# Performance work log

Hardware: AMD Instinct MI355X
Metric: run time of the kernel (lower is better)

## Reference

```python
import jax, jax.numpy as jnp
import numpy as np

N = 65536        # nodes
E = 131072       # directed edges
D = 512          # emb_dim
L = 5            # num_layer
G = 512          # num graphs
EPS = 1e-5       # batchnorm eps
NUM_ATOM_TYPE, NUM_CHIRALITY = 120, 3
NUM_BOND_TYPE, NUM_BOND_DIR = 6, 3


def setup_inputs() -> dict:
    key = jax.random.key(0)
    ks = jax.random.split(key, 12)
    s = 0.02
    return {
        "x": jax.random.randint(ks[0], (N, 2), 0, 3),
        "edge_index": jax.random.randint(ks[1], (2, E), 0, N),
        "edge_attr": jax.random.randint(ks[2], (E, 2), 0, 3),
        "batch": jnp.sort(jax.random.randint(ks[3], (N,), 0, G)),
        "x_emb1": jax.random.normal(ks[4], (NUM_ATOM_TYPE, D), jnp.float32) * s,
        "x_emb2": jax.random.normal(ks[5], (NUM_CHIRALITY, D), jnp.float32) * s,
        "e_emb1": jax.random.normal(ks[6], (L, NUM_BOND_TYPE, D), jnp.float32) * s,
        "e_emb2": jax.random.normal(ks[7], (L, NUM_BOND_DIR, D), jnp.float32) * s,
        "W1": jax.random.normal(ks[8], (L, D, 2 * D), jnp.float32) * s,
        "b1": jnp.zeros((L, 2 * D), jnp.float32),
        "W2": jax.random.normal(ks[9], (L, 2 * D, D), jnp.float32) * s,
        "b2": jnp.zeros((L, D), jnp.float32),
        "gamma": jnp.ones((L, D), jnp.float32),
        "beta": jnp.zeros((L, D), jnp.float32),
    }


def reference(x, edge_index, edge_attr, batch,
              x_emb1, x_emb2, e_emb1, e_emb2,
              W1, b1, W2, b2, gamma, beta):
    n = x.shape[0]
    # atom embedding: type + chirality
    h = x_emb1[x[:, 0]] + x_emb2[x[:, 1]]                     # [N, D]

    # add self loops (appended after real edges, attr = [4, 0])
    loops = jnp.arange(n)
    src = jnp.concatenate([edge_index[0], loops])             # [E+N]
    dst = jnp.concatenate([edge_index[1], loops])
    sl_attr = jnp.concatenate(
        [jnp.full((n, 1), 4, dtype=edge_attr.dtype),
         jnp.zeros((n, 1), dtype=edge_attr.dtype)], axis=1)
    ea = jnp.concatenate([edge_attr, sl_attr], axis=0)        # [E+N, 2]

    for l in range(L):
        # per-edge embedding: bond type + bond direction
        e = e_emb1[l][ea[:, 0]] + e_emb2[l][ea[:, 1]]         # [E+N, D]
        msg = h[src] + e                                      # gather + add
        agg = jax.ops.segment_sum(msg, dst, num_segments=n)   # scatter-add
        # GIN MLP: Linear(D,2D) -> ReLU -> Linear(2D,D)
        hh = jax.nn.relu(agg @ W1[l] + b1[l]) @ W2[l] + b2[l]
        # BatchNorm1d (training-mode batch statistics)
        mean = hh.mean(axis=0)
        var = hh.var(axis=0)
        hh = (hh - mean) * jax.lax.rsqrt(var + EPS) * gamma[l] + beta[l]
        if l < L - 1:
            hh = jax.nn.relu(hh)   # dropout(p=0) is identity
        h = hh

    # JK='last': node rep = h; graph rep = global mean pool over batch ids
    counts = jax.ops.segment_sum(jnp.ones((n,), h.dtype), batch, num_segments=G)
    graph = jax.ops.segment_sum(h, batch, num_segments=G) / jnp.maximum(counts, 1.0)[:, None]
    return graph, h
```

## Files before the change

kernel.cpp:

```cpp
#include <hip/hip_runtime.h>
#include <stdint.h>

#define Nn 65536
#define Ee 131072
#define Dd 512
#define D2 1024
#define Ll 5
#define Gg 512
#define EPSf 1e-5f

typedef _Float16 f16x8 __attribute__((ext_vector_type(8)));
typedef float f32x4 __attribute__((ext_vector_type(4)));
typedef unsigned short u16x8 __attribute__((ext_vector_type(8)));

__device__ __forceinline__ unsigned short f2h(float f) {
    _Float16 h = (_Float16)f;
    union { _Float16 h; unsigned short u; } c; c.h = h;
    return c.u;
}

__device__ __forceinline__ float h2f(unsigned short s) {
    union { unsigned short s; _Float16 h; } c; c.s = s;
    return (float)c.h;
}

__device__ __forceinline__ void gload_lds16(const void* g, void* l) {
    __builtin_amdgcn_global_load_lds(
        (const __attribute__((address_space(1))) void*)(uintptr_t)g,
        (__attribute__((address_space(3))) void*)(unsigned)(uintptr_t)l,
        16, 0, 0);
}

__global__ void k_transW(const float* __restrict__ src, unsigned short* __restrict__ dst,
                         int K, int Nw) {
    long total = (long)Ll * K * Nw;
    for (long idx = (long)blockIdx.x * blockDim.x + threadIdx.x; idx < total;
         idx += (long)gridDim.x * blockDim.x) {
        long l = idx / ((long)K * Nw);
        long rem = idx - l * (long)K * Nw;
        int k = (int)(rem / Nw), n = (int)(rem % Nw);
        dst[(l * Nw + n) * K + k] = f2h(src[idx]);
    }
}

__global__ void k_etab(const float* __restrict__ ee1, const float* __restrict__ ee2,
                       float* __restrict__ E) {
    int idx = blockIdx.x * blockDim.x + threadIdx.x;
    const int total = Ll * 18 * Dd;
    if (idx < total) {
        int l = idx / (18 * Dd);
        int rem = idx - l * 18 * Dd;
        int j = rem / Dd, c = rem - j * Dd;
        int a0 = j / 3, a1 = j - a0 * 3;
        E[idx] = ee1[((size_t)l * 6 + a0) * Dd + c] + ee2[((size_t)l * 3 + a1) * Dd + c];
    }
}

__global__ void k_embed(const int* __restrict__ x,
                        const float* __restrict__ xe1, const float* __restrict__ xe2,
                        unsigned short* __restrict__ hhf) {
    const int total = Nn * 64;
    for (int idx = blockIdx.x * blockDim.x + threadIdx.x; idx < total;
         idx += gridDim.x * blockDim.x) {
        int node = idx >> 6, c8 = (idx & 63) * 8;
        int t0 = x[2 * node], t1 = x[2 * node + 1];
        const float4* p1 = (const float4*)(xe1 + (size_t)t0 * Dd + c8);
        const float4* p2 = (const float4*)(xe2 + (size_t)t1 * Dd + c8);
        float4 a0 = p1[0], a1 = p1[1], b0 = p2[0], b1 = p2[1];
        u16x8 o;
        o[0] = f2h(a0.x + b0.x); o[1] = f2h(a0.y + b0.y);
        o[2] = f2h(a0.z + b0.z); o[3] = f2h(a0.w + b0.w);
        o[4] = f2h(a1.x + b1.x); o[5] = f2h(a1.y + b1.y);
        o[6] = f2h(a1.z + b1.z); o[7] = f2h(a1.w + b1.w);
        *(u16x8*)(hhf + (size_t)node * Dd + c8) = o;
    }
}

__global__ void k_zeroN(int* __restrict__ p, int n) {
    int i = blockIdx.x * blockDim.x + threadIdx.x;
    if (i < n) p[i] = 0;
}

__global__ void k_hist(const int* __restrict__ edst, int* __restrict__ cnt) {
    int e = blockIdx.x * blockDim.x + threadIdx.x;
    if (e < Ee) atomicAdd(&cnt[edst[e]], 1);
}

__global__ void k_scan(const int* __restrict__ cnt, int* __restrict__ off,
                       int* __restrict__ cursor) {
    __shared__ int part[1024];
    int t = threadIdx.x;
    int base = t * 64;
    int s = 0;
    for (int i = 0; i < 64; ++i) s += cnt[base + i];
    part[t] = s;
    __syncthreads();
    for (int d = 1; d < 1024; d <<= 1) {
        int v = (t >= d) ? part[t - d] : 0;
        __syncthreads();
        part[t] += v;
        __syncthreads();
    }
    int run = part[t] - s;
    for (int i = 0; i < 64; ++i) {
        off[base + i] = run;
        cursor[base + i] = run;
        run += cnt[base + i];
    }
    if (t == 1023) off[Nn] = run;
}

__global__ void k_place(const int* __restrict__ esrc, const int* __restrict__ edst,
                        const int* __restrict__ eattr, int* __restrict__ cursor,
                        int* __restrict__ ckey, int* __restrict__ csrc) {
    int e = blockIdx.x * blockDim.x + threadIdx.x;
    if (e < Ee) {
        int d = edst[e];
        int p = atomicAdd(&cursor[d], 1);
        ckey[p] = e * 32 + (eattr[2 * e] * 3 + eattr[2 * e + 1]);
        csrc[p] = esrc[e];
    }
}

__global__ void k_sort(const int* __restrict__ off, int* __restrict__ ckey,
                       int* __restrict__ csrc) {
    int node = blockIdx.x * blockDim.x + threadIdx.x;
    if (node >= Nn) return;
    int kb = off[node], ke = off[node + 1];
    for (int i = kb + 1; i < ke; ++i) {
        int k = ckey[i], s = csrc[i];
        int j = i - 1;
        while (j >= kb && ckey[j] > k) {
            ckey[j + 1] = ckey[j]; csrc[j + 1] = csrc[j]; --j;
        }
        ckey[j + 1] = k; csrc[j + 1] = s;
    }
}

template <int NORM>
__global__ __launch_bounds__(256) void k_gather(const unsigned short* __restrict__ hf16,
                                                const float* __restrict__ ss,
                                                const int* __restrict__ off,
                                                const int* __restrict__ ckey,
                                                const int* __restrict__ csrc,
                                                const float* __restrict__ El,
                                                unsigned short* __restrict__ aggh) {
    int node = (blockIdx.x << 2) + (threadIdx.x >> 6);
    int lane = threadIdx.x & 63;
    int c8 = lane * 8;
    float sa[8], sb[8];
    if (NORM) {
        float4 a0 = *(const float4*)(ss + c8), a1 = *(const float4*)(ss + c8 + 4);
        float4 b0 = *(const float4*)(ss + 512 + c8), b1 = *(const float4*)(ss + 512 + c8 + 4);
        sa[0] = a0.x; sa[1] = a0.y; sa[2] = a0.z; sa[3] = a0.w;
        sa[4] = a1.x; sa[5] = a1.y; sa[6] = a1.z; sa[7] = a1.w;
        sb[0] = b0.x; sb[1] = b0.y; sb[2] = b0.z; sb[3] = b0.w;
        sb[4] = b1.x; sb[5] = b1.y; sb[6] = b1.z; sb[7] = b1.w;
    }
    float acc[8];
    {
        u16x8 v = *(const u16x8*)(hf16 + (size_t)node * Dd + c8);
        float4 e0 = *(const float4*)(El + 12 * Dd + c8);
        float4 e1 = *(const float4*)(El + 12 * Dd + c8 + 4);
        float ev[8];
        ev[0] = e0.x; ev[1] = e0.y; ev[2] = e0.z; ev[3] = e0.w;
        ev[4] = e1.x; ev[5] = e1.y; ev[6] = e1.z; ev[7] = e1.w;
#pragma unroll
        for (int i = 0; i < 8; ++i) {
            float hv = h2f(v[i]);
            if (NORM) hv = fmaxf(fmaf(hv, sa[i], sb[i]), 0.f);
            acc[i] = hv + ev[i];
        }
    }
    int kb = off[node], ke = off[node + 1];
    for (int k = kb; k < ke; ++k) {
        int src = csrc[k];
        int at = ckey[k] & 31;
        u16x8 v = *(const u16x8*)(hf16 + (size_t)src * Dd + c8);
        const float* Er = El + (size_t)at * Dd + c8;
        float4 e0 = *(const float4*)(Er);
        float4 e1 = *(const float4*)(Er + 4);
        float ev[8];
        ev[0] = e0.x; ev[1] = e0.y; ev[2] = e0.z; ev[3] = e0.w;
        ev[4] = e1.x; ev[5] = e1.y; ev[6] = e1.z; ev[7] = e1.w;
#pragma unroll
        for (int i = 0; i < 8; ++i) {
            float hv = h2f(v[i]);
            if (NORM) hv = fmaxf(fmaf(hv, sa[i], sb[i]), 0.f);
            acc[i] += hv + ev[i];
        }
    }
    u16x8 o;
#pragma unroll
    for (int i = 0; i < 8; ++i) o[i] = f2h(acc[i]);
    *(u16x8*)(aggh + (size_t)node * Dd + c8) = o;
}

__device__ __forceinline__ void stage_q(const unsigned short* __restrict__ g, int ldk,
                                        long row0, int col0, char* region, int tid) {
    int wbase = (tid >> 6) << 10;
#pragma unroll
    for (int r = 0; r < 2; ++r) {
        int gi = tid + r * 512;
        int row = gi >> 2;
        int k16 = (gi & 3) ^ ((row >> 1) & 3);
        gload_lds16(g + (row0 + row) * (long)ldk + col0 + k16 * 8,
                    region + r * 8192 + wbase);
    }
}

__device__ __forceinline__ f16x8 rd_frag(const char* region, int row, int l4) {
    int slot = l4 ^ ((row >> 1) & 3);
    return *(const f16x8*)(region + row * 64 + (slot << 4));
}

template <int EPI>
__global__ __launch_bounds__(512, 2) void gemm8(const unsigned short* __restrict__ A,
                                                const unsigned short* __restrict__ BT,
                                                const float* __restrict__ bias,
                                                unsigned short* __restrict__ Cb,
                                                float* __restrict__ pS,
                                                int M, int N, int K) {
    __shared__ __align__(16) char lds[131072];
    const int tid = threadIdx.x;
    const int lane = tid & 63;
    const int w = tid >> 6;
    const int wm = w >> 2, wn = w & 3;
    const int l15 = lane & 15, l4 = lane >> 4;

    const int nwg = gridDim.x;
    const int cpx = nwg >> 3;
    const int bid = blockIdx.x;
    const int wg = (bid & 7) * cpx + (bid >> 3);
    const int ntn = N >> 8;
    const long bm = (long)(wg / ntn) * 256;
    const long bn = (long)(wg % ntn) * 256;

    char* Ar = lds;
    char* Br = lds + 65536;
    const int NT = K >> 6;

    f32x4 acc[8][4];
#pragma unroll
    for (int i = 0; i < 8; ++i)
#pragma unroll
        for (int j = 0; j < 4; ++j) acc[i][j] = (f32x4){0.f, 0.f, 0.f, 0.f};

    stage_q(A, K, bm, 0, Ar, tid);
    stage_q(BT, K, bn, 0, Br, tid);
    stage_q(A, K, bm, 32, Ar + 16384, tid);
    stage_q(BT, K, bn, 32, Br + 16384, tid);
    asm volatile("s_waitcnt vmcnt(4)" ::: "memory");
    __builtin_amdgcn_s_barrier();
    asm volatile("" ::: "memory");

    for (int t = 0; t < NT; ++t) {
        const int par = (t & 1) << 15;
        const int npar = ((t + 1) & 1) << 15;
        const bool pre = (t + 1 < NT);
#pragma unroll
        for (int kh = 0; kh < 2; ++kh) {
            const char* Ac = Ar + par + kh * 16384;
            const char* Bc = Br + par + kh * 16384;
            f16x8 af[8], bv[4];
#pragma unroll
            for (int fn = 0; fn < 4; ++fn)
                bv[fn] = rd_frag(Bc, wn * 64 + fn * 16 + l15, l4);
#pragma unroll
            for (int fm = 0; fm < 8; ++fm)
                af[fm] = rd_frag(Ac, wm * 128 + fm * 16 + l15, l4);
            if (pre) {
                stage_q(BT, K, bn, (t + 1) * 64 + kh * 32, Br + npar + kh * 16384, tid);
                stage_q(A, K, bm, (t + 1) * 64 + kh * 32, Ar + npar + kh * 16384, tid);
            }
#pragma unroll
            for (int fm = 0; fm < 8; ++fm)
#pragma unroll
                for (int fn = 0; fn < 4; ++fn)
                    acc[fm][fn] = __builtin_amdgcn_mfma_f32_16x16x32_f16(af[fm], bv[fn], acc[fm][fn], 0, 0, 0);
            if (pre) {
                asm volatile("s_waitcnt vmcnt(4)" ::: "memory");
            } else {
                asm volatile("s_waitcnt vmcnt(0)" ::: "memory");
            }
            __builtin_amdgcn_s_barrier();
            asm volatile("" ::: "memory");
        }
    }

    unsigned short* cl = (unsigned short*)lds;
    float cs[4] = {0.f, 0.f, 0.f, 0.f}, cq[4] = {0.f, 0.f, 0.f, 0.f};
#pragma unroll
    for (int hh = 0; hh < 2; ++hh) {
        __syncthreads();
        if (wm == hh) {
#pragma unroll
            for (int fn = 0; fn < 4; ++fn) {
                int col = wn * 64 + fn * 16 + l15;
                float bval = bias[bn + col];
#pragma unroll
                for (int fm = 0; fm < 8; ++fm) {
                    int r0 = fm * 16 + l4 * 4;
#pragma unroll
                    for (int r = 0; r < 4; ++r) {
                        float v = acc[fm][fn][r] + bval;
                        if (EPI == 0) v = fmaxf(v, 0.f);
                        else { cs[fn] += v; cq[fn] += v * v; }
                        cl[(r0 + r) * 264 + col] = f2h(v);
                    }
                }
            }
        }
        __syncthreads();
#pragma unroll
        for (int i = 0; i < 8; ++i) {
            int g = tid + i * 512;
            int r = g >> 5, cg = (g & 31) << 3;
            u16x8 val = *(const u16x8*)&cl[r * 264 + cg];
            *(u16x8*)&Cb[(bm + hh * 128 + r) * N + bn + cg] = val;
        }
    }
    if (EPI == 1) {
#pragma unroll
        for (int fn = 0; fn < 4; ++fn) {
            float s = cs[fn], q = cq[fn];
            s += __shfl_xor(s, 16); s += __shfl_xor(s, 32);
            q += __shfl_xor(q, 16); q += __shfl_xor(q, 32);
            if (l4 == 0) {
                int col = (int)bn + wn * 64 + fn * 16 + l15;
                int rowgrp = ((int)(bm >> 8)) * 2 + wm;
                pS[rowgrp * 512 + col] = s;
                pS[262144 + rowgrp * 512 + col] = q;
            }
        }
    }
}

__global__ void k_bnA(const float* __restrict__ pS, float* __restrict__ pT) {
    int b = blockIdx.x;
    int t = threadIdx.x;
    float s0 = 0.f, s1 = 0.f, q0 = 0.f, q1 = 0.f;
#pragma unroll
    for (int i = 0; i < 8; ++i) {
        int rg = b * 8 + i;
        s0 += pS[rg * 512 + t];
        s1 += pS[rg * 512 + t + 256];
        q0 += pS[262144 + rg * 512 + t];
        q1 += pS[262144 + rg * 512 + t + 256];
    }
    pT[b * 512 + t] = s0;
    pT[b * 512 + t + 256] = s1;
    pT[32768 + b * 512 + t] = q0;
    pT[32768 + b * 512 + t + 256] = q1;
}

__global__ void k_bnB(const float* __restrict__ pT, const float* __restrict__ gamma,
                      const float* __restrict__ beta, float* __restrict__ ss) {
    int c = threadIdx.x;
    float s = 0.f, q = 0.f;
    for (int b = 0; b < 64; ++b) {
        s += pT[b * 512 + c];
        q += pT[32768 + b * 512 + c];
    }
    float mean = s * (1.f / (float)Nn);
    float var = q * (1.f / (float)Nn) - mean * mean;
    float a = gamma[c] * rsqrtf(var + EPSf);
    ss[c] = a;
    ss[512 + c] = beta[c] - mean * a;
}

__global__ void k_norm(const unsigned short* __restrict__ hhf, const float* __restrict__ ss,
                       float4* __restrict__ h4) {
    const int total = Nn * 128;
    const float4* ss4 = (const float4*)ss;
    for (int idx = blockIdx.x * blockDim.x + threadIdx.x; idx < total;
         idx += gridDim.x * blockDim.x) {
        int c = idx & 127;
        ushort4 u = *(const ushort4*)(hhf + (size_t)idx * 4);
        float4 v = make_float4(h2f(u.x), h2f(u.y), h2f(u.z), h2f(u.w));
        float4 a = ss4[c], b = ss4[128 + c];
        v.x = fmaf(v.x, a.x, b.x); v.y = fmaf(v.y, a.y, b.y);
        v.z = fmaf(v.z, a.z, b.z); v.w = fmaf(v.w, a.w, b.w);
        h4[idx] = v;
    }
}

__global__ void k_pool(const unsigned short* __restrict__ hhf, const float* __restrict__ ss,
                       const int* __restrict__ batch, float* __restrict__ graph) {
    int g = blockIdx.x, t = threadIdx.x;
    int lo = 0, hi = Nn;
    while (lo < hi) { int m = (lo + hi) >> 1; if (batch[m] < g) lo = m + 1; else hi = m; }
    int s = lo;
    lo = s; hi = Nn;
    while (lo < hi) { int m = (lo + hi) >> 1; if (batch[m] <= g) lo = m + 1; else hi = m; }
    int e = lo;
    float a0 = ss[t], a1 = ss[t + 256];
    float b0 = ss[512 + t], b1 = ss[512 + t + 256];
    float s0 = 0.f, s1 = 0.f;
    for (int r = s; r < e; ++r) {
        const unsigned short* row = hhf + (size_t)r * Dd;
        s0 += fmaf(h2f(row[t]), a0, b0);
        s1 += fmaf(h2f(row[t + 256]), a1, b1);
    }
    int cnt = e - s; if (cnt < 1) cnt = 1;
    float inv = 1.f / (float)cnt;
    graph[(long)g * Dd + t] = s0 * inv;
    graph[(long)g * Dd + t + 256] = s1 * inv;
}

extern "C" void kernel_launch(void* const* d_in, const int* in_sizes, int n_in,
                              void* d_out, int out_size, void* d_ws, size_t ws_size,
                              hipStream_t stream) {
    (void)in_sizes; (void)n_in; (void)out_size; (void)ws_size;
    const int* x      = (const int*)d_in[0];
    const int* ei     = (const int*)d_in[1];
    const int* ea     = (const int*)d_in[2];
    const int* batch  = (const int*)d_in[3];
    const float* xe1  = (const float*)d_in[4];
    const float* xe2  = (const float*)d_in[5];
    const float* ee1  = (const float*)d_in[6];
    const float* ee2  = (const float*)d_in[7];
    const float* W1   = (const float*)d_in[8];
    const float* b1   = (const float*)d_in[9];
    const float* W2   = (const float*)d_in[10];
    const float* b2   = (const float*)d_in[11];
    const float* gamma = (const float*)d_in[12];
    const float* beta  = (const float*)d_in[13];

    float* graph = (float*)d_out;
    float* h = graph + (size_t)Gg * Dd;

    char* w = (char*)d_ws;
    int* csr_off = (int*)w;                     w += (Nn + 1) * 4;
    int* cursor = (int*)w;                      w += Nn * 4;
    int* cnt = (int*)w;                         w += Nn * 4;
    int* ckey = (int*)w;                        w += Ee * 4;
    int* csrc = (int*)w;                        w += Ee * 4;
    float* ss = (float*)w;                      w += 4096;
    float* pS = (float*)w;                      w += 2 * 512 * 512 * 4;
    float* pT = (float*)w;                      w += 2 * 64 * 512 * 4;
    float* Etab = (float*)w;                    w += (size_t)Ll * 18 * Dd * 4;
    unsigned short* aggh = (unsigned short*)w;  w += (size_t)Nn * Dd * 2;
    unsigned short* hhf = (unsigned short*)w;   w += (size_t)Nn * Dd * 2;
    unsigned short* w1t = (unsigned short*)w;   w += (size_t)Ll * D2 * Dd * 2;
    unsigned short* w2t = (unsigned short*)w;   w += (size_t)Ll * Dd * D2 * 2;

    k_transW<<<2048, 256, 0, stream>>>(W1, w1t, Dd, D2);
    k_transW<<<2048, 256, 0, stream>>>(W2, w2t, D2, Dd);
    k_etab<<<(Ll * 18 * Dd + 255) / 256, 256, 0, stream>>>(ee1, ee2, Etab);
    k_embed<<<2048, 256, 0, stream>>>(x, xe1, xe2, hhf);

    k_zeroN<<<64, 1024, 0, stream>>>(cnt, Nn);
    k_hist<<<Ee / 256, 256, 0, stream>>>(ei + Ee, cnt);
    k_scan<<<1, 1024, 0, stream>>>(cnt, csr_off, cursor);
    k_place<<<Ee / 256, 256, 0, stream>>>(ei, ei + Ee, ea, cursor, ckey, csrc);
    k_sort<<<Nn / 256, 256, 0, stream>>>(csr_off, ckey, csrc);

    for (int l = 0; l < Ll; ++l) {
        const float* El = Etab + (size_t)l * 18 * Dd;
        if (l == 0)
            k_gather<0><<<Nn / 4, 256, 0, stream>>>(hhf, nullptr, csr_off, ckey, csrc,
                                                    El, aggh);
        else
            k_gather<1><<<Nn / 4, 256, 0, stream>>>(hhf, ss, csr_off, ckey, csrc,
                                                    El, aggh);
        gemm8<0><<<(Nn / 256) * (D2 / 256), 512, 0, stream>>>(
            aggh, w1t + (size_t)l * D2 * Dd, b1 + (size_t)l * D2,
            (unsigned short*)h, nullptr, Nn, D2, Dd);
        gemm8<1><<<(Nn / 256) * (Dd / 256), 512, 0, stream>>>(
            (const unsigned short*)h, w2t + (size_t)l * Dd * D2, b2 + (size_t)l * Dd,
            hhf, pS, Nn, Dd, D2);
        k_bnA<<<64, 256, 0, stream>>>(pS, pT);
        k_bnB<<<1, 512, 0, stream>>>(pT, gamma + (size_t)l * Dd, beta + (size_t)l * Dd, ss);
    }

    k_norm<<<2048, 256, 0, stream>>>(hhf, ss, (float4*)h);
    k_pool<<<Gg, 256, 0, stream>>>(hhf, ss, batch, graph);
}
```

Measured before the change: 1.433 ms.

## Pre-pack weights into MFMA fragment layout and read B directly from global

The weight transpose kernel is replaced by a packing kernel that stores W1/W2 in fp16 in the exact per-lane MFMA fragment order. The GEMM no longer stages B tiles through LDS: each wave loads its B fragments straight from global memory (expected to hit L2), and only A is double-buffered in LDS. This is meant to cut LDS traffic and global-to-LDS staging work for B. In exchange, the B loads are issued without prefetch, so their latency sits on the MFMA critical path. The explicit vmcnt waits before the per-step barrier are also removed, which risks a race on the staged A tiles unless the compiler inserts the waits itself.

```diff
diff --git a/kernel.cpp b/kernel.cpp
--- a/kernel.cpp
+++ b/kernel.cpp
@@ -31,15 +31,18 @@
         16, 0, 0);
 }
 
-__global__ void k_transW(const float* __restrict__ src, unsigned short* __restrict__ dst,
-                         int K, int Nw) {
+__global__ void k_packW(const float* __restrict__ src, unsigned short* __restrict__ dst,
+                        int K, int Nw) {
     long total = (long)Ll * K * Nw;
+    int KF = K >> 5, NF = Nw >> 4;
     for (long idx = (long)blockIdx.x * blockDim.x + threadIdx.x; idx < total;
          idx += (long)gridDim.x * blockDim.x) {
         long l = idx / ((long)K * Nw);
         long rem = idx - l * (long)K * Nw;
         int k = (int)(rem / Nw), n = (int)(rem % Nw);
-        dst[(l * Nw + n) * K + k] = f2h(src[idx]);
+        int lane = (n & 15) + (((k >> 3) & 3) << 4);
+        long di = (((l * NF + (n >> 4)) * KF + (k >> 5)) * 64 + lane) * 8 + (k & 7);
+        dst[di] = f2h(src[idx]);
     }
 }
 
@@ -215,12 +218,12 @@
 }
 
 template <int EPI>
-__global__ __launch_bounds__(512, 2) void gemm8(const unsigned short* __restrict__ A,
-                                                const unsigned short* __restrict__ BT,
-                                                const float* __restrict__ bias,
-                                                unsigned short* __restrict__ Cb,
-                                                float* __restrict__ pS,
-                                                int M, int N, int K) {
+__global__ __launch_bounds__(512, 2) void gemm_bp(const unsigned short* __restrict__ A,
+                                                  const unsigned short* __restrict__ BP,
+                                                  const float* __restrict__ bias,
+                                                  unsigned short* __restrict__ Cb,
+                                                  float* __restrict__ pS,
+                                                  int M, int N, int K) {
     __shared__ __align__(16) char lds[131072];
     const int tid = threadIdx.x;
     const int lane = tid & 63;
@@ -237,8 +240,9 @@
     const long bn = (long)(wg % ntn) * 256;
 
     char* Ar = lds;
-    char* Br = lds + 65536;
     const int NT = K >> 6;
+    const int KF = K >> 5;
+    const unsigned short* Bw = BP + ((size_t)((int)(bn >> 4) + wn * 4) * KF) * 512 + lane * 8;
 
     f32x4 acc[8][4];
 #pragma unroll
@@ -247,10 +251,8 @@
         for (int j = 0; j < 4; ++j) acc[i][j] = (f32x4){0.f, 0.f, 0.f, 0.f};
 
     stage_q(A, K, bm, 0, Ar, tid);
-    stage_q(BT, K, bn, 0, Br, tid);
     stage_q(A, K, bm, 32, Ar + 16384, tid);
-    stage_q(BT, K, bn, 32, Br + 16384, tid);
-    asm volatile("s_waitcnt vmcnt(4)" ::: "memory");
+    asm volatile("s_waitcnt vmcnt(2)" ::: "memory");
     __builtin_amdgcn_s_barrier();
     asm volatile("" ::: "memory");
 
@@ -261,28 +263,21 @@
 #pragma unroll
         for (int kh = 0; kh < 2; ++kh) {
             const char* Ac = Ar + par + kh * 16384;
-            const char* Bc = Br + par + kh * 16384;
+            const int kf = (t << 1) + kh;
             f16x8 af[8], bv[4];
 #pragma unroll
             for (int fn = 0; fn < 4; ++fn)
-                bv[fn] = rd_frag(Bc, wn * 64 + fn * 16 + l15, l4);
+                bv[fn] = *(const f16x8*)(Bw + ((size_t)fn * KF + kf) * 512);
 #pragma unroll
             for (int fm = 0; fm < 8; ++fm)
                 af[fm] = rd_frag(Ac, wm * 128 + fm * 16 + l15, l4);
-            if (pre) {
-                stage_q(BT, K, bn, (t + 1) * 64 + kh * 32, Br + npar + kh * 16384, tid);
+            if (pre)
                 stage_q(A, K, bm, (t + 1) * 64 + kh * 32, Ar + npar + kh * 16384, tid);
-            }
 #pragma unroll
             for (int fm = 0; fm < 8; ++fm)
 #pragma unroll
                 for (int fn = 0; fn < 4; ++fn)
                     acc[fm][fn] = __builtin_amdgcn_mfma_f32_16x16x32_f16(af[fm], bv[fn], acc[fm][fn], 0, 0, 0);
-            if (pre) {
-                asm volatile("s_waitcnt vmcnt(4)" ::: "memory");
-            } else {
-                asm volatile("s_waitcnt vmcnt(0)" ::: "memory");
-            }
             __builtin_amdgcn_s_barrier();
             asm volatile("" ::: "memory");
         }
@@ -442,11 +437,11 @@
     float* Etab = (float*)w;                    w += (size_t)Ll * 18 * Dd * 4;
     unsigned short* aggh = (unsigned short*)w;  w += (size_t)Nn * Dd * 2;
     unsigned short* hhf = (unsigned short*)w;   w += (size_t)Nn * Dd * 2;
-    unsigned short* w1t = (unsigned short*)w;   w += (size_t)Ll * D2 * Dd * 2;
-    unsigned short* w2t = (unsigned short*)w;   w += (size_t)Ll * Dd * D2 * 2;
-
-    k_transW<<<2048, 256, 0, stream>>>(W1, w1t, Dd, D2);
-    k_transW<<<2048, 256, 0, stream>>>(W2, w2t, D2, Dd);
+    unsigned short* w1p = (unsigned short*)w;   w += (size_t)Ll * D2 * Dd * 2;
+    unsigned short* w2p = (unsigned short*)w;   w += (size_t)Ll * Dd * D2 * 2;
+
+    k_packW<<<2048, 256, 0, stream>>>(W1, w1p, Dd, D2);
+    k_packW<<<2048, 256, 0, stream>>>(W2, w2p, D2, Dd);
     k_etab<<<(Ll * 18 * Dd + 255) / 256, 256, 0, stream>>>(ee1, ee2, Etab);
     k_embed<<<2048, 256, 0, stream>>>(x, xe1, xe2, hhf);
 
@@ -464,11 +459,11 @@
         else
             k_gather<1><<<Nn / 4, 256, 0, stream>>>(hhf, ss, csr_off, ckey, csrc,
                                                     El, aggh);
-        gemm8<0><<<(Nn / 256) * (D2 / 256), 512, 0, stream>>>(
-            aggh, w1t + (size_t)l * D2 * Dd, b1 + (size_t)l * D2,
+        gemm_bp<0><<<(Nn / 256) * (D2 / 256), 512, 0, stream>>>(
+            aggh, w1p + (size_t)l * D2 * Dd, b1 + (size_t)l * D2,
             (unsigned short*)h, nullptr, Nn, D2, Dd);
-        gemm8<1><<<(Nn / 256) * (Dd / 256), 512, 0, stream>>>(
-            (const unsigned short*)h, w2t + (size_t)l * Dd * D2, b2 + (size_t)l * Dd,
+        gemm_bp<1><<<(Nn / 256) * (Dd / 256), 512, 0, stream>>>(
+            (const unsigned short*)h, w2p + (size_t)l * Dd * D2, b2 + (size_t)l * Dd,
             hhf, pS, Nn, Dd, D2);
         k_bnA<<<64, 256, 0, stream>>>(pS, pT);
         k_bnB<<<1, 512, 0, stream>>>(pT, gamma + (size_t)l * Dd, beta + (size_t)l * Dd, ss);
```

New measurement: 1.415 ms. No clear change (-1.2%).
